# Kernel tuning notes

Measured on AMD Instinct MI355X. Metric: run time of the kernel, lower is better.

Reference implementation:

```python
import jax, jax.numpy as jnp
import numpy as np

N_CLOSEST = 16
OBJECTNESS_THRESH = 0.75


def _masked_softmax(att, mask):
    # softmax over axis 1 restricted to mask; rows with empty mask -> all zeros
    neg = jnp.where(mask, att, -jnp.inf)
    m = jnp.max(neg, axis=1, keepdims=True)
    m = jnp.where(jnp.isfinite(m), m, 0.0)
    e = jnp.where(mask, jnp.exp(att - m), 0.0)
    d = jnp.sum(e, axis=1, keepdims=True)
    return jnp.where(d > 0, e / jnp.maximum(d, 1e-30), 0.0)


def _forward(aggregated_vote_features, ref_obj_features, objectness_scores,
             ref_center_label, aggregated_vote_xyz, emb_table, init_emb,
             W_enc_att, b_enc_att, W_dec_att, b_dec_att, w_full_att, b_full_att,
             W_ih, b_ih, W_hh, b_hh, W_init_h, b_init_h, W_init_c, b_init_c,
             W_fbeta, b_fbeta, W_fc, b_fc, lang_indices, lang_len):
    B, K, VD = aggregated_vote_features.shape
    T = lang_indices.shape[1]

    # --- objectness + distance (top-k closest) masking ---
    objness = jax.nn.softmax(objectness_scores, axis=-1)[:, :, -1]      # [B,K]
    omask = objness > OBJECTNESS_THRESH
    dist = jnp.linalg.norm(ref_center_label[:, None, :] - aggregated_vote_xyz, axis=2)
    dist = jnp.where(omask, dist, jnp.inf)
    closest = -jax.lax.top_k(-dist, N_CLOSEST)[0]                        # k smallest
    max_d = jnp.max(closest, axis=1, keepdims=True)
    object_mask = omask & (dist <= max_d)                                # [B,K]

    enc = aggregated_vote_features                                       # [B,K,VD]
    init_in = jnp.concatenate([enc.mean(axis=1), ref_obj_features], axis=1)
    h0 = init_in @ W_init_h.T + b_init_h                                 # [B,D]
    c0 = init_in @ W_init_c.T + b_init_c

    # encoder attention projection is constant over timesteps
    att1 = jnp.einsum('bkv,av->bka', enc, W_enc_att) + b_enc_att         # [B,K,A]

    # teacher-forcing inputs: <unk> init embedding then caption embeddings
    E = init_emb.shape[-1]
    emb = jnp.concatenate(
        [jnp.broadcast_to(init_emb, (B, E))[:, None, :], emb_table[lang_indices]],
        axis=1)                                                          # [B,T+1,E]
    emb_steps = jnp.swapaxes(emb[:, :T], 0, 1)                           # [T,B,E]
    t_steps = jnp.arange(T)

    def step(carry, xs):
        h, c = carry
        emb_t, t = xs
        # attention
        att2 = h @ W_dec_att.T + b_dec_att                               # [B,A]
        att = jax.nn.relu(att1 + att2[:, None, :]) @ w_full_att + b_full_att[0]  # [B,K]
        alpha = _masked_softmax(att, object_mask)
        awe = jnp.einsum('bkv,bk->bv', enc, alpha)                       # [B,VD]
        gate = jax.nn.sigmoid(h @ W_fbeta.T + b_fbeta)
        awe = gate * awe
        # LSTMCell (torch gate order i,f,g,o)
        x = jnp.concatenate([emb_t, awe, ref_obj_features], axis=1)      # [B,E+VD+OD]
        gates = x @ W_ih.T + b_ih + h @ W_hh.T + b_hh
        i, f, g, o = jnp.split(gates, 4, axis=1)
        c_new = jax.nn.sigmoid(f) * c + jax.nn.sigmoid(i) * jnp.tanh(g)
        h_new = jax.nn.sigmoid(o) * jnp.tanh(c_new)
        # only samples with length > t are decoded (masked equivalent of batch_size_t)
        active = (t < lang_len)[:, None]
        preds = jnp.where(active, h_new @ W_fc.T + b_fc, 0.0)            # [B,V]
        alpha_o = jnp.where(active, alpha, 0.0)
        h = jnp.where(active, h_new, h)
        c = jnp.where(active, c_new, c)
        return (h, c), (preds, alpha_o)

    _, (preds_seq, alpha_seq) = jax.lax.scan(step, (h0, c0), (emb_steps, t_steps))
    predictions = jnp.transpose(preds_seq, (1, 2, 0))                    # [B,V,T]
    alphas = jnp.transpose(alpha_seq, (1, 0, 2))                         # [B,T,K]
    return predictions, alphas, object_mask


def setup_inputs() -> dict:
    key = jax.random.key(0)
    ks = jax.random.split(key, 20)
    B, K, VD, OD, E, A, D, V, T = 128, 128, 128, 256, 300, 512, 512, 4000, 32
    ENC = VD + OD

    def rn(k, shape, s=1.0):
        return jax.random.normal(k, shape, jnp.float32) * s

    return {
        'aggregated_vote_features': rn(ks[0], (B, K, VD)),
        'ref_obj_features': rn(ks[1], (B, OD)),
        'objectness_scores': rn(ks[2], (B, K, 2)),
        'ref_center_label': rn(ks[3], (B, 3)),
        'aggregated_vote_xyz': rn(ks[4], (B, K, 3)),
        'lang_indices': jax.random.randint(ks[5], (B, T), 0, V),
        'lang_len': jax.random.randint(ks[6], (B,), 1, T + 1),
        'emb_table': rn(ks[7], (V, E), 0.1),
        'init_emb': rn(ks[8], (1, E), 0.1),
        'W_enc_att': rn(ks[9], (A, VD), 0.05), 'b_enc_att': jnp.zeros((A,)),
        'W_dec_att': rn(ks[10], (A, D), 0.05), 'b_dec_att': jnp.zeros((A,)),
        'w_full_att': rn(ks[11], (A,), 0.05), 'b_full_att': jnp.zeros((1,)),
        'W_ih': rn(ks[12], (4 * D, E + ENC), 0.05), 'b_ih': jnp.zeros((4 * D,)),
        'W_hh': rn(ks[13], (4 * D, D), 0.05), 'b_hh': jnp.zeros((4 * D,)),
        'W_init_h': rn(ks[14], (D, ENC), 0.05), 'b_init_h': jnp.zeros((D,)),
        'W_init_c': rn(ks[15], (D, ENC), 0.05), 'b_init_c': jnp.zeros((D,)),
        'W_fbeta': rn(ks[16], (VD, D), 0.05), 'b_fbeta': jnp.zeros((VD,)),
        'W_fc': rn(ks[17], (V, D), 0.1), 'b_fc': jnp.zeros((V,)),
    }


def reference(aggregated_vote_features, ref_obj_features, objectness_scores,
              ref_center_label, aggregated_vote_xyz, lang_indices, lang_len,
              emb_table, init_emb, W_enc_att, b_enc_att, W_dec_att, b_dec_att,
              w_full_att, b_full_att, W_ih, b_ih, W_hh, b_hh, W_init_h, b_init_h,
              W_init_c, b_init_c, W_fbeta, b_fbeta, W_fc, b_fc):
    return _forward(aggregated_vote_features, ref_obj_features, objectness_scores,
                    ref_center_label, aggregated_vote_xyz, emb_table, init_emb,
                    W_enc_att, b_enc_att, W_dec_att, b_dec_att, w_full_att, b_full_att,
                    W_ih, b_ih, W_hh, b_hh, W_init_h, b_init_h, W_init_c, b_init_c,
                    W_fbeta, b_fbeta, W_fc, b_fc, lang_indices, lang_len)
```

## Files before the change

### kernel.cpp

```cpp
#include <hip/hip_runtime.h>
#include <hip/hip_bf16.h>
#include <math.h>

#define XKTOT 1196
#define XKP   1216

typedef unsigned short u16;
typedef short bf16x8 __attribute__((ext_vector_type(8)));
typedef float f32x4 __attribute__((ext_vector_type(4)));

static __device__ __forceinline__ float sigmoidf_(float x){ return 1.f/(1.f+expf(-x)); }
static __device__ __forceinline__ u16 f2bf(float x){ __hip_bfloat16 h = __float2bfloat16(x); return *reinterpret_cast<u16*>(&h); }
static __device__ __forceinline__ float bf2f(u16 u){ __hip_bfloat16 h; *reinterpret_cast<u16*>(&h) = u; return __bfloat162float(h); }

__global__ __launch_bounds__(256) void k_transpose(const float* __restrict__ in,
                                                   float* __restrict__ out, int R, int C) {
  __shared__ float tile[32][33];
  int c0 = blockIdx.x * 32, r0 = blockIdx.y * 32;
  int tx = threadIdx.x & 31, ty = threadIdx.x >> 5;
  for (int i = 0; i < 32; i += 8) {
    int r = r0 + ty + i, c = c0 + tx;
    tile[ty + i][tx] = (r < R && c < C) ? in[(size_t)r * C + c] : 0.f;
  }
  __syncthreads();
  for (int i = 0; i < 32; i += 8) {
    int c = c0 + ty + i, r = r0 + tx;
    if (c < C && r < R) out[(size_t)c * R + r] = tile[tx][ty + i];
  }
}

__global__ __launch_bounds__(256) void k_cvt(const float* __restrict__ in,
                                             u16* __restrict__ out, int n) {
  for (int i = blockIdx.x * 256 + threadIdx.x; i < n; i += gridDim.x * 256)
    out[i] = f2bf(in[i]);
}

__global__ __launch_bounds__(256) void k_wcat_split(const float* __restrict__ W_ih,
                                                    const float* __restrict__ W_hh,
                                                    u16* __restrict__ Whi,
                                                    u16* __restrict__ Wlo) {
  int np = blockIdx.x;
  int d = np >> 2, g = np & 3;
  int j = g * 512 + d;
  for (int c = threadIdx.x; c < XKP; c += 256) {
    float v;
    if (c < 684)        v = W_ih[(size_t)j * 684 + c];
    else if (c < 1196)  v = W_hh[(size_t)j * 512 + (c - 684)];
    else                v = 0.f;
    u16 hi = f2bf(v);
    u16 lo = f2bf(v - bf2f(hi));
    Whi[(size_t)np * XKP + c] = hi;
    Wlo[(size_t)np * XKP + c] = lo;
  }
}

__global__ __launch_bounds__(128) void k_mask(const float* __restrict__ objs,
                                              const float* __restrict__ rcl,
                                              const float* __restrict__ avx,
                                              const float* __restrict__ enc,
                                              float* __restrict__ maskf,
                                              float* __restrict__ encmean,
                                              float* __restrict__ out_mask) {
  int b = blockIdx.x, k = threadIdx.x;
  __shared__ float dsh[128];
  __shared__ float maxd;
  float s0 = objs[(size_t)(b * 128 + k) * 2 + 0];
  float s1 = objs[(size_t)(b * 128 + k) * 2 + 1];
  float mx = fmaxf(s0, s1);
  float e0 = expf(s0 - mx), e1 = expf(s1 - mx);
  float p  = e1 / (e0 + e1);
  bool om  = p > 0.75f;
  float dx = rcl[b * 3 + 0] - avx[(size_t)(b * 128 + k) * 3 + 0];
  float dy = rcl[b * 3 + 1] - avx[(size_t)(b * 128 + k) * 3 + 1];
  float dz = rcl[b * 3 + 2] - avx[(size_t)(b * 128 + k) * 3 + 2];
  float dist = sqrtf(dx * dx + dy * dy + dz * dz);
  float dm = om ? dist : INFINITY;
  dsh[k] = dm;
  __syncthreads();
  float v = dm; int clt = 0, cle = 0;
  for (int j = 0; j < 128; j++) { float o = dsh[j]; clt += (o < v); cle += (o <= v); }
  if (clt < 16 && cle >= 16) maxd = v;
  __syncthreads();
  bool msk = om && (dm <= maxd);
  maskf[b * 128 + k]    = msk ? 1.f : 0.f;
  out_mask[b * 128 + k] = msk ? 1.f : 0.f;
  float s = 0.f;
  for (int kk = 0; kk < 128; kk++) s += enc[(size_t)(b * 128 + kk) * 128 + k];
  encmean[b * 128 + k] = s * (1.f / 128.f);
}

__global__ __launch_bounds__(512) void k_init(const float* __restrict__ encm,
                                              const float* __restrict__ rof,
                                              const float* __restrict__ wihT,
                                              const float* __restrict__ wicT,
                                              const float* __restrict__ bh,
                                              const float* __restrict__ bc,
                                              float* __restrict__ h, float* __restrict__ c,
                                              u16* __restrict__ hb16) {
  int b = blockIdx.x, d = threadIdx.x;
  __shared__ float xin[384];
  if (d < 128) xin[d] = encm[b * 128 + d];
  else if (d < 384) xin[d] = rof[(size_t)b * 256 + (d - 128)];
  __syncthreads();
  float ah = bh[d], ac = bc[d];
  for (int i = 0; i < 384; i++) {
    float x = xin[i];
    ah += x * wihT[(size_t)i * 512 + d];
    ac += x * wicT[(size_t)i * 512 + d];
  }
  size_t idx = (size_t)b * 512 + d;
  h[idx] = ah;
  c[idx] = ac;
  hb16[idx] = f2bf(ah);
}

__global__ __launch_bounds__(256) void k_att1m(const u16* __restrict__ enc16,
                                               const u16* __restrict__ We16,
                                               const float* __restrict__ b_enc,
                                               float* __restrict__ att1) {
  int w = threadIdx.x >> 6, lane = threadIdx.x & 63;
  int gw = blockIdx.x * 4 + w;
  int nt = gw & 15, mt = gw >> 4;
  int m0 = mt * 32, n0 = nt * 32;
  int rc = lane & 15, kb = lane >> 4;
  const bf16x8* a0 = (const bf16x8*)(enc16 + (size_t)(m0 + rc) * 128) + kb;
  const bf16x8* a1 = (const bf16x8*)(enc16 + (size_t)(m0 + 16 + rc) * 128) + kb;
  const bf16x8* b0 = (const bf16x8*)(We16 + (size_t)(n0 + rc) * 128) + kb;
  const bf16x8* b1 = (const bf16x8*)(We16 + (size_t)(n0 + 16 + rc) * 128) + kb;
  f32x4 z = {0.f, 0.f, 0.f, 0.f};
  f32x4 acc00 = z, acc01 = z, acc10 = z, acc11 = z;
#pragma unroll
  for (int kk = 0; kk < 4; kk++) {
    bf16x8 av0 = a0[kk * 4], av1 = a1[kk * 4];
    bf16x8 bv0 = b0[kk * 4], bv1 = b1[kk * 4];
    acc00 = __builtin_amdgcn_mfma_f32_16x16x32_bf16(av0, bv0, acc00, 0, 0, 0);
    acc01 = __builtin_amdgcn_mfma_f32_16x16x32_bf16(av0, bv1, acc01, 0, 0, 0);
    acc10 = __builtin_amdgcn_mfma_f32_16x16x32_bf16(av1, bv0, acc10, 0, 0, 0);
    acc11 = __builtin_amdgcn_mfma_f32_16x16x32_bf16(av1, bv1, acc11, 0, 0, 0);
  }
  int col = lane & 15, rbase = (lane >> 4) * 4;
#pragma unroll
  for (int r = 0; r < 4; r++) {
    int r0g = m0 + rbase + r;
    att1[(size_t)r0g * 512 + n0 + col]        = acc00[r] + b_enc[n0 + col];
    att1[(size_t)r0g * 512 + n0 + 16 + col]   = acc01[r] + b_enc[n0 + 16 + col];
    att1[(size_t)(r0g + 16) * 512 + n0 + col]      = acc10[r] + b_enc[n0 + col];
    att1[(size_t)(r0g + 16) * 512 + n0 + 16 + col] = acc11[r] + b_enc[n0 + 16 + col];
  }
}

__global__ __launch_bounds__(512) void k_step_att(
    const float* __restrict__ att1, const float* __restrict__ h,
    const float* __restrict__ wdT, const float* __restrict__ b_dec,
    const float* __restrict__ wfull, const float* __restrict__ bfull,
    const float* __restrict__ enc, const float* __restrict__ maskf,
    const float* __restrict__ wfbT, const float* __restrict__ b_fbeta,
    const float* __restrict__ rof, const float* __restrict__ embt,
    const float* __restrict__ iemb, const int* __restrict__ lidx,
    const int* __restrict__ llen, u16* __restrict__ Xhi, u16* __restrict__ Xlo,
    float* __restrict__ alphas_out, int t) {
  int b = blockIdx.x, tid = threadIdx.x;
  __shared__ float hs[512], att2[512], wf[512], attk[128], alph[128], awes[128];
  __shared__ float red1[2], red2[2];
  hs[tid] = h[(size_t)b * 512 + tid];
  wf[tid] = wfull[tid];
  __syncthreads();
  {
    float acc = b_dec[tid];
    for (int i = 0; i < 512; i++) acc += hs[i] * wdT[(size_t)i * 512 + tid];
    att2[tid] = acc;
  }
  __syncthreads();
  int k = tid >> 2, j = tid & 3;
  {
    const float4* a1 = (const float4*)(att1 + (size_t)(b * 128 + k) * 512 + j * 128);
    float s = 0.f;
#pragma unroll 4
    for (int i = 0; i < 32; i++) {
      float4 v = a1[i];
      int base = j * 128 + i * 4;
      s += fmaxf(v.x + att2[base + 0], 0.f) * wf[base + 0];
      s += fmaxf(v.y + att2[base + 1], 0.f) * wf[base + 1];
      s += fmaxf(v.z + att2[base + 2], 0.f) * wf[base + 2];
      s += fmaxf(v.w + att2[base + 3], 0.f) * wf[base + 3];
    }
    s += __shfl_xor(s, 1);
    s += __shfl_xor(s, 2);
    if (j == 0) attk[k] = s + bfull[0];
  }
  __syncthreads();
  float mk = 0.f, av = 0.f;
  if (tid < 128) { mk = maskf[b * 128 + tid]; av = attk[tid]; }
  float nv = (tid < 128 && mk != 0.f) ? av : -INFINITY;
  float wm = nv;
#pragma unroll
  for (int o = 32; o > 0; o >>= 1) wm = fmaxf(wm, __shfl_xor(wm, o));
  if (tid < 128 && (tid & 63) == 0) red1[tid >> 6] = wm;
  __syncthreads();
  float m = fmaxf(red1[0], red1[1]);
  float e = 0.f;
  if (tid < 128 && mk != 0.f) e = expf(av - m);
  float sred = e;
#pragma unroll
  for (int o = 32; o > 0; o >>= 1) sred += __shfl_xor(sred, o);
  if (tid < 128 && (tid & 63) == 0) red2[tid >> 6] = sred;
  __syncthreads();
  float dsum = red2[0] + red2[1];
  float alpha = (dsum > 0.f) ? e / fmaxf(dsum, 1e-30f) : 0.f;
  int active = t < llen[b];
  if (tid < 128) {
    alph[tid] = alpha;
    alphas_out[(size_t)(b * 32 + t) * 128 + tid] = active ? alpha : 0.f;
  }
  __syncthreads();
  float awe_v = 0.f;
  if (tid < 128) {
    for (int kk = 0; kk < 128; kk++)
      awe_v += alph[kk] * enc[(size_t)(b * 128 + kk) * 128 + tid];
  }
  {
    int v = tid >> 2;
    float g = 0.f;
    for (int ii = 0; ii < 128; ii++) {
      int i = j * 128 + ii;
      g += hs[i] * wfbT[(size_t)i * 128 + v];
    }
    g += __shfl_xor(g, 1);
    g += __shfl_xor(g, 2);
    if (j == 0) attk[v] = sigmoidf_(g + b_fbeta[v]);
  }
  __syncthreads();
  if (tid < 128) awes[tid] = awe_v * attk[tid];
  __syncthreads();
  const float* esrc = (t == 0) ? iemb : (embt + (size_t)lidx[b * 32 + (t - 1)] * 300);
  for (int c = tid; c < XKP; c += 512) {
    float val;
    if (c < 300)       val = esrc[c];
    else if (c < 428)  val = awes[c - 300];
    else if (c < 684)  val = rof[(size_t)b * 256 + (c - 428)];
    else if (c < 1196) val = hs[c - 684];
    else               val = 0.f;
    u16 hi = f2bf(val);
    Xhi[(size_t)b * XKP + c] = hi;
    Xlo[(size_t)b * XKP + c] = f2bf(val - bf2f(hi));
  }
}

__global__ __launch_bounds__(256) void k_gates(const u16* __restrict__ Xhi,
                                               const u16* __restrict__ Xlo,
                                               const u16* __restrict__ Whi,
                                               const u16* __restrict__ Wlo,
                                               const float* __restrict__ b_ih,
                                               const float* __restrict__ b_hh,
                                               const int* __restrict__ llen,
                                               float* __restrict__ h, float* __restrict__ c,
                                               u16* __restrict__ hb16, int t) {
  int w = threadIdx.x >> 6, lane = threadIdx.x & 63;
  int mt = blockIdx.x >> 5;
  int nt = (blockIdx.x & 31) * 4 + w;
  int m0 = mt * 16, n0 = nt * 16;
  int rc = lane & 15, kb = lane >> 4;
  const bf16x8* aHi = (const bf16x8*)(Xhi + (size_t)(m0 + rc) * XKP) + kb;
  const bf16x8* aLo = (const bf16x8*)(Xlo + (size_t)(m0 + rc) * XKP) + kb;
  const bf16x8* bHi = (const bf16x8*)(Whi + (size_t)(n0 + rc) * XKP) + kb;
  const bf16x8* bLo = (const bf16x8*)(Wlo + (size_t)(n0 + rc) * XKP) + kb;
  f32x4 acc = {0.f, 0.f, 0.f, 0.f};
#pragma unroll 2
  for (int kk = 0; kk < 38; kk++) {
    bf16x8 ah = aHi[kk * 4], al = aLo[kk * 4];
    bf16x8 bh = bHi[kk * 4], bl = bLo[kk * 4];
    acc = __builtin_amdgcn_mfma_f32_16x16x32_bf16(ah, bh, acc, 0, 0, 0);
    acc = __builtin_amdgcn_mfma_f32_16x16x32_bf16(al, bh, acc, 0, 0, 0);
    acc = __builtin_amdgcn_mfma_f32_16x16x32_bf16(ah, bl, acc, 0, 0, 0);
  }
  __shared__ float tile[4][16][17];
#pragma unroll
  for (int r = 0; r < 4; r++) tile[w][(lane >> 4) * 4 + r][lane & 15] = acc[r];
  __syncthreads();
  int lb = lane & 15, ld = lane >> 4;
  int b = m0 + lb, d = nt * 4 + ld;
  if (t < llen[b]) {
    float g4[4];
#pragma unroll
    for (int g = 0; g < 4; g++) {
      int jj = g * 512 + d;
      g4[g] = tile[w][lb][ld * 4 + g] + b_ih[jj] + b_hh[jj];
    }
    float i_ = sigmoidf_(g4[0]);
    float f_ = sigmoidf_(g4[1]);
    float gg = tanhf(g4[2]);
    float o_ = sigmoidf_(g4[3]);
    size_t idx = (size_t)b * 512 + d;
    float cn = f_ * c[idx] + i_ * gg;
    float hn = o_ * tanhf(cn);
    c[idx] = cn;
    h[idx] = hn;
    hb16[idx] = f2bf(hn);
  }
}

__global__ __launch_bounds__(256) void k_fc(const u16* __restrict__ hb16,
                                            const u16* __restrict__ Wfc16,
                                            const float* __restrict__ b_fc,
                                            const int* __restrict__ llen,
                                            float* __restrict__ dst, int t, int direct) {
  int w = threadIdx.x >> 6, lane = threadIdx.x & 63;
  int gw = blockIdx.x * 4 + w;
  int mt = gw & 7, nt = gw >> 3;
  int m0 = mt * 16, n0 = nt * 16;
  int rc = lane & 15, kb = lane >> 4;
  const bf16x8* aP = (const bf16x8*)(hb16 + (size_t)(m0 + rc) * 512) + kb;
  const bf16x8* bP = (const bf16x8*)(Wfc16 + (size_t)(n0 + rc) * 512) + kb;
  f32x4 acc = {0.f, 0.f, 0.f, 0.f};
#pragma unroll 4
  for (int kk = 0; kk < 16; kk++)
    acc = __builtin_amdgcn_mfma_f32_16x16x32_bf16(aP[kk * 4], bP[kk * 4], acc, 0, 0, 0);
  int col = lane & 15, rbase = (lane >> 4) * 4;
  int v = n0 + col;
  float bias = b_fc[v];
#pragma unroll
  for (int r = 0; r < 4; r++) {
    int b = m0 + rbase + r;
    float val = (t < llen[b]) ? (acc[r] + bias) : 0.f;
    if (direct) dst[((size_t)b * 4000 + v) * 32 + t] = val;
    else        dst[((size_t)(t * 128 + b)) * 4000 + v] = val;
  }
}

__global__ __launch_bounds__(256) void k_out_tr(const float* __restrict__ predsT,
                                                float* __restrict__ out) {
  __shared__ float tile[32][33];
  int b = blockIdx.y, v0 = blockIdx.x * 32;
  int tx = threadIdx.x & 31, ty = threadIdx.x >> 5;
  for (int i = 0; i < 32; i += 8) {
    int tt = ty + i;
    tile[tt][tx] = predsT[((size_t)tt * 128 + b) * 4000 + v0 + tx];
  }
  __syncthreads();
  for (int i = 0; i < 32; i += 8) {
    int v = v0 + ty + i;
    out[((size_t)b * 4000 + v) * 32 + tx] = tile[tx][ty + i];
  }
}

extern "C" void kernel_launch(void* const* d_in, const int* in_sizes, int n_in,
                              void* d_out, int out_size, void* d_ws, size_t ws_size,
                              hipStream_t stream) {
  (void)in_sizes; (void)n_in; (void)out_size;
  const float* avf   = (const float*)d_in[0];
  const float* rof   = (const float*)d_in[1];
  const float* objs  = (const float*)d_in[2];
  const float* rcl   = (const float*)d_in[3];
  const float* avx   = (const float*)d_in[4];
  const int*   lidx  = (const int*)d_in[5];
  const int*   llen  = (const int*)d_in[6];
  const float* embt  = (const float*)d_in[7];
  const float* iemb  = (const float*)d_in[8];
  const float* W_enc = (const float*)d_in[9];
  const float* b_enc = (const float*)d_in[10];
  const float* W_dec = (const float*)d_in[11];
  const float* b_dec = (const float*)d_in[12];
  const float* wfull = (const float*)d_in[13];
  const float* bfull = (const float*)d_in[14];
  const float* W_ih  = (const float*)d_in[15];
  const float* b_ih  = (const float*)d_in[16];
  const float* W_hh  = (const float*)d_in[17];
  const float* b_hh  = (const float*)d_in[18];
  const float* W_inh = (const float*)d_in[19];
  const float* b_inh = (const float*)d_in[20];
  const float* W_inc = (const float*)d_in[21];
  const float* b_inc = (const float*)d_in[22];
  const float* W_fb  = (const float*)d_in[23];
  const float* b_fb  = (const float*)d_in[24];
  const float* W_fc  = (const float*)d_in[25];
  const float* b_fc  = (const float*)d_in[26];

  float* ws = (float*)d_ws;
  size_t f = 0;
  auto A8 = [&](size_t n) { size_t o = f; f += (n + 63) & ~(size_t)63; return o; };
  float* att1  = ws + A8((size_t)128 * 128 * 512);
  float* wdT   = ws + A8(512 * 512);
  float* wihT  = ws + A8(384 * 512);
  float* wicT  = ws + A8(384 * 512);
  float* wfbT  = ws + A8(512 * 128);
  float* hbuf  = ws + A8(128 * 512);
  float* cbuf  = ws + A8(128 * 512);
  float* maskf = ws + A8(128 * 128);
  float* encm  = ws + A8(128 * 128);
  u16*   Xhi   = (u16*)(ws + A8((size_t)128 * XKP / 2));
  u16*   Xlo   = (u16*)(ws + A8((size_t)128 * XKP / 2));
  u16*   WcatHi= (u16*)(ws + A8((size_t)2048 * XKP / 2));
  u16*   WcatLo= (u16*)(ws + A8((size_t)2048 * XKP / 2));
  u16*   enc16 = (u16*)(ws + A8((size_t)128 * 128 * 128 / 2));
  u16*   We16  = (u16*)(ws + A8((size_t)512 * 128 / 2));
  u16*   Wfc16 = (u16*)(ws + A8((size_t)4000 * 512 / 2));
  u16*   hb16  = (u16*)(ws + A8((size_t)128 * 512 / 2));
  float* predsT= ws + A8((size_t)32 * 128 * 4000);
  bool useT = ws_size >= f * sizeof(float);

  float* out_pred  = (float*)d_out;
  float* out_alpha = out_pred + (size_t)16384000;
  float* out_mask  = out_alpha + (size_t)524288;

  k_transpose<<<dim3(16, 16), 256, 0, stream>>>(W_dec, wdT, 512, 512);
  k_transpose<<<dim3(12, 16), 256, 0, stream>>>(W_inh, wihT, 512, 384);
  k_transpose<<<dim3(12, 16), 256, 0, stream>>>(W_inc, wicT, 512, 384);
  k_transpose<<<dim3(16, 4),  256, 0, stream>>>(W_fb, wfbT, 128, 512);
  k_wcat_split<<<2048, 256, 0, stream>>>(W_ih, W_hh, WcatHi, WcatLo);
  k_cvt<<<2048, 256, 0, stream>>>(avf, enc16, 128 * 128 * 128);
  k_cvt<<<256,  256, 0, stream>>>(W_enc, We16, 512 * 128);
  k_cvt<<<2048, 256, 0, stream>>>(W_fc, Wfc16, 4000 * 512);
  k_mask<<<128, 128, 0, stream>>>(objs, rcl, avx, avf, maskf, encm, out_mask);
  k_init<<<128, 512, 0, stream>>>(encm, rof, wihT, wicT, b_inh, b_inc, hbuf, cbuf, hb16);
  k_att1m<<<2048, 256, 0, stream>>>(enc16, We16, b_enc, att1);

  for (int t = 0; t < 32; t++) {
    k_step_att<<<128, 512, 0, stream>>>(att1, hbuf, wdT, b_dec, wfull, bfull,
        avf, maskf, wfbT, b_fb, rof, embt, iemb, lidx, llen, Xhi, Xlo, out_alpha, t);
    k_gates<<<256, 256, 0, stream>>>(Xhi, Xlo, WcatHi, WcatLo, b_ih, b_hh, llen,
                                     hbuf, cbuf, hb16, t);
    k_fc<<<500, 256, 0, stream>>>(hb16, Wfc16, b_fc, llen,
                                  useT ? predsT : out_pred, t, useT ? 0 : 1);
  }
  if (useT) k_out_tr<<<dim3(125, 128), 256, 0, stream>>>(predsT, out_pred);
}
```

Baseline: 2.435 ms.

## Fuse per-timestep decoder kernels into one cooperative persistent kernel with grid syncs

Replaces the 96 per-step launches (attention, gates, fc) and the final transpose with a single cooperative kernel of 256 blocks. Each step is separated by grid.sync. The decoder-attention projection now runs as a bf16 MFMA GEMM instead of a scalar FP32 loop. The fc output of step t-1 is overlapped with the att2 GEMM of step t. This cuts launch overhead and reduces the work done per block, but it relies on grid-wide barriers, runs at limited occupancy, and lowers att2 precision to bf16.

```diff
diff --git a/kernel.cpp b/kernel.cpp
--- a/kernel.cpp
+++ b/kernel.cpp
@@ -1,9 +1,11 @@
 #include <hip/hip_runtime.h>
 #include <hip/hip_bf16.h>
+#include <hip/hip_cooperative_groups.h>
 #include <math.h>
 
-#define XKTOT 1196
-#define XKP   1216
+namespace cg = cooperative_groups;
+
+#define XKP 1216
 
 typedef unsigned short u16;
 typedef short bf16x8 __attribute__((ext_vector_type(8)));
@@ -149,197 +151,253 @@
   }
 }
 
-__global__ __launch_bounds__(512) void k_step_att(
-    const float* __restrict__ att1, const float* __restrict__ h,
-    const float* __restrict__ wdT, const float* __restrict__ b_dec,
-    const float* __restrict__ wfull, const float* __restrict__ bfull,
-    const float* __restrict__ enc, const float* __restrict__ maskf,
-    const float* __restrict__ wfbT, const float* __restrict__ b_fbeta,
-    const float* __restrict__ rof, const float* __restrict__ embt,
-    const float* __restrict__ iemb, const int* __restrict__ lidx,
-    const int* __restrict__ llen, u16* __restrict__ Xhi, u16* __restrict__ Xlo,
-    float* __restrict__ alphas_out, int t) {
-  int b = blockIdx.x, tid = threadIdx.x;
-  __shared__ float hs[512], att2[512], wf[512], attk[128], alph[128], awes[128];
-  __shared__ float red1[2], red2[2];
-  hs[tid] = h[(size_t)b * 512 + tid];
-  wf[tid] = wfull[tid];
-  __syncthreads();
+struct DecArgs {
+  const float* att1;
+  const u16*   Wdec16;
+  const float* b_dec;
+  const float* wfull;
+  const float* bfull;
+  const float* avf;
+  const float* maskf;
+  const float* wfbT;
+  const float* b_fb;
+  const float* rof;
+  const float* embt;
+  const float* iemb;
+  const int*   lidx;
+  const int*   llen;
+  const u16*   WcatHi;
+  const u16*   WcatLo;
+  const float* b_ih;
+  const float* b_hh;
+  const u16*   Wfc16;
+  const float* b_fc;
+  float* hbuf; float* cbuf; u16* hb16;
+  u16* Xhi; u16* Xlo;
+  float* att2s;
+  float* predsT;
+  float* out_alpha;
+  float* out_pred;
+  int direct;
+};
+
+__global__ __launch_bounds__(256) void k_decode(DecArgs A) {
+  cg::grid_group grid = cg::this_grid();
+  const int tid = threadIdx.x;
+  const int w = tid >> 6, lane = tid & 63;
+  const int gw = blockIdx.x * 4 + w;
+  const int rc = lane & 15, kb = lane >> 4;
+
+  __shared__ float hs[512], a2s[512], wf[512];
+  __shared__ float attk[128], alph[128], gts[128], awes[128];
+  __shared__ float red[8];
+  __shared__ float ttile[32][33];
+
+  for (int t = 0; t < 32; ++t) {
+    if (gw < 256) {
+      int mt = gw & 7, nt = gw >> 3;
+      int m0 = mt * 16, n0 = nt * 16;
+      const bf16x8* aP = (const bf16x8*)(A.hb16 + (size_t)(m0 + rc) * 512) + kb;
+      const bf16x8* bP = (const bf16x8*)(A.Wdec16 + (size_t)(n0 + rc) * 512) + kb;
+      f32x4 acc = {0.f, 0.f, 0.f, 0.f};
+#pragma unroll
+      for (int kk = 0; kk < 16; kk++)
+        acc = __builtin_amdgcn_mfma_f32_16x16x32_bf16(aP[kk * 4], bP[kk * 4], acc, 0, 0, 0);
+      int col = lane & 15, rb = (lane >> 4) * 4;
+      float bias = A.b_dec[n0 + col];
+#pragma unroll
+      for (int r = 0; r < 4; r++)
+        A.att2s[(size_t)(m0 + rb + r) * 512 + n0 + col] = acc[r] + bias;
+    } else if (t > 0) {
+      int tp = t - 1;
+      for (int tile = gw - 256; tile < 2000; tile += 768) {
+        int mt = tile & 7, nt = tile >> 3;
+        int m0 = mt * 16, n0 = nt * 16;
+        const bf16x8* aP = (const bf16x8*)(A.hb16 + (size_t)(m0 + rc) * 512) + kb;
+        const bf16x8* bP = (const bf16x8*)(A.Wfc16 + (size_t)(n0 + rc) * 512) + kb;
+        f32x4 acc = {0.f, 0.f, 0.f, 0.f};
+#pragma unroll
+        for (int kk = 0; kk < 16; kk++)
+          acc = __builtin_amdgcn_mfma_f32_16x16x32_bf16(aP[kk * 4], bP[kk * 4], acc, 0, 0, 0);
+        int col = lane & 15, rb = (lane >> 4) * 4;
+        int v = n0 + col;
+        float bias = A.b_fc[v];
+#pragma unroll
+        for (int r = 0; r < 4; r++) {
+          int b = m0 + rb + r;
+          float val = (tp < A.llen[b]) ? (acc[r] + bias) : 0.f;
+          if (A.direct) A.out_pred[((size_t)b * 4000 + v) * 32 + tp] = val;
+          else          A.predsT[((size_t)(tp * 128 + b)) * 4000 + v] = val;
+        }
+      }
+    }
+    grid.sync();
+
+    if (blockIdx.x < 128) {
+      int b = blockIdx.x;
+      hs[tid] = A.hbuf[(size_t)b * 512 + tid];
+      hs[tid + 256] = A.hbuf[(size_t)b * 512 + 256 + tid];
+      a2s[tid] = A.att2s[(size_t)b * 512 + tid];
+      a2s[tid + 256] = A.att2s[(size_t)b * 512 + 256 + tid];
+      wf[tid] = A.wfull[tid];
+      wf[tid + 256] = A.wfull[tid + 256];
+      __syncthreads();
+      {
+        int k = tid >> 1, half = tid & 1;
+        const float4* a1 = (const float4*)(A.att1 + ((size_t)(b * 128 + k)) * 512 + half * 256);
+        float s = 0.f;
+#pragma unroll 4
+        for (int i = 0; i < 64; i++) {
+          float4 v = a1[i];
+          int base = half * 256 + i * 4;
+          s += fmaxf(v.x + a2s[base + 0], 0.f) * wf[base + 0];
+          s += fmaxf(v.y + a2s[base + 1], 0.f) * wf[base + 1];
+          s += fmaxf(v.z + a2s[base + 2], 0.f) * wf[base + 2];
+          s += fmaxf(v.w + a2s[base + 3], 0.f) * wf[base + 3];
+        }
+        s += __shfl_xor(s, 1);
+        if (half == 0) attk[k] = s + A.bfull[0];
+      }
+      __syncthreads();
+      float mk = 0.f, av = 0.f;
+      if (tid < 128) { mk = A.maskf[b * 128 + tid]; av = attk[tid]; }
+      float nv = (tid < 128 && mk != 0.f) ? av : -INFINITY;
+      float wm = nv;
+#pragma unroll
+      for (int o = 32; o > 0; o >>= 1) wm = fmaxf(wm, __shfl_xor(wm, o));
+      if (tid < 128 && lane == 0) red[w] = wm;
+      __syncthreads();
+      float m = fmaxf(red[0], red[1]);
+      float e = (tid < 128 && mk != 0.f) ? expf(av - m) : 0.f;
+      float sr = e;
+#pragma unroll
+      for (int o = 32; o > 0; o >>= 1) sr += __shfl_xor(sr, o);
+      if (tid < 128 && lane == 0) red[4 + w] = sr;
+      __syncthreads();
+      float dsum = red[4] + red[5];
+      float alpha = (dsum > 0.f) ? e / fmaxf(dsum, 1e-30f) : 0.f;
+      int active = t < A.llen[b];
+      if (tid < 128) {
+        alph[tid] = alpha;
+        A.out_alpha[((size_t)b * 32 + t) * 128 + tid] = active ? alpha : 0.f;
+      }
+      __syncthreads();
+      float awe_v = 0.f;
+      if (tid < 128) {
+        for (int kk = 0; kk < 128; kk++)
+          awe_v += alph[kk] * A.avf[((size_t)b * 128 + kk) * 128 + tid];
+      }
+      {
+        int v = tid >> 1, half = tid & 1;
+        float g = 0.f;
+        for (int ii = 0; ii < 256; ii++) {
+          int i = half * 256 + ii;
+          g += hs[i] * A.wfbT[(size_t)i * 128 + v];
+        }
+        g += __shfl_xor(g, 1);
+        if (half == 0) gts[v] = sigmoidf_(g + A.b_fb[v]);
+      }
+      __syncthreads();
+      if (tid < 128) awes[tid] = awe_v * gts[tid];
+      __syncthreads();
+      const float* esrc = (t == 0) ? A.iemb : (A.embt + (size_t)A.lidx[b * 32 + (t - 1)] * 300);
+      for (int c = tid; c < XKP; c += 256) {
+        float val;
+        if (c < 300)       val = esrc[c];
+        else if (c < 428)  val = awes[c - 300];
+        else if (c < 684)  val = A.rof[(size_t)b * 256 + (c - 428)];
+        else if (c < 1196) val = hs[c - 684];
+        else               val = 0.f;
+        u16 hi = f2bf(val);
+        A.Xhi[(size_t)b * XKP + c] = hi;
+        A.Xlo[(size_t)b * XKP + c] = f2bf(val - bf2f(hi));
+      }
+    }
+    grid.sync();
+
+    {
+      int mt = gw >> 7, ntp = gw & 127;
+      int m0 = mt * 16, n0 = ntp * 16;
+      const bf16x8* aHi = (const bf16x8*)(A.Xhi + (size_t)(m0 + rc) * XKP) + kb;
+      const bf16x8* aLo = (const bf16x8*)(A.Xlo + (size_t)(m0 + rc) * XKP) + kb;
+      const bf16x8* bHi = (const bf16x8*)(A.WcatHi + (size_t)(n0 + rc) * XKP) + kb;
+      const bf16x8* bLo = (const bf16x8*)(A.WcatLo + (size_t)(n0 + rc) * XKP) + kb;
+      f32x4 acc = {0.f, 0.f, 0.f, 0.f};
+#pragma unroll 2
+      for (int kk = 0; kk < 38; kk++) {
+        bf16x8 ah = aHi[kk * 4], al = aLo[kk * 4];
+        bf16x8 bh = bHi[kk * 4], bl = bLo[kk * 4];
+        acc = __builtin_amdgcn_mfma_f32_16x16x32_bf16(ah, bh, acc, 0, 0, 0);
+        acc = __builtin_amdgcn_mfma_f32_16x16x32_bf16(al, bh, acc, 0, 0, 0);
+        acc = __builtin_amdgcn_mfma_f32_16x16x32_bf16(ah, bl, acc, 0, 0, 0);
+      }
+      int col = lane & 15;
+      int d = ntp * 4 + (col >> 2);
+      int baseL = lane & ~3;
+#pragma unroll
+      for (int r = 0; r < 4; r++) {
+        int b = m0 + (lane >> 4) * 4 + r;
+        float g0 = __shfl(acc[r], baseL + 0);
+        float g1 = __shfl(acc[r], baseL + 1);
+        float g2 = __shfl(acc[r], baseL + 2);
+        float g3 = __shfl(acc[r], baseL + 3);
+        if ((lane & 3) == 0 && t < A.llen[b]) {
+          float i_ = sigmoidf_(g0 + A.b_ih[d]        + A.b_hh[d]);
+          float f_ = sigmoidf_(g1 + A.b_ih[512 + d]  + A.b_hh[512 + d]);
+          float gg = tanhf   (g2 + A.b_ih[1024 + d] + A.b_hh[1024 + d]);
+          float o_ = sigmoidf_(g3 + A.b_ih[1536 + d] + A.b_hh[1536 + d]);
+          size_t idx = (size_t)b * 512 + d;
+          float cn = f_ * A.cbuf[idx] + i_ * gg;
+          float hn = o_ * tanhf(cn);
+          A.cbuf[idx] = cn;
+          A.hbuf[idx] = hn;
+          A.hb16[idx] = f2bf(hn);
+        }
+      }
+    }
+    grid.sync();
+  }
+
   {
-    float acc = b_dec[tid];
-    for (int i = 0; i < 512; i++) acc += hs[i] * wdT[(size_t)i * 512 + tid];
-    att2[tid] = acc;
-  }
-  __syncthreads();
-  int k = tid >> 2, j = tid & 3;
-  {
-    const float4* a1 = (const float4*)(att1 + (size_t)(b * 128 + k) * 512 + j * 128);
-    float s = 0.f;
-#pragma unroll 4
-    for (int i = 0; i < 32; i++) {
-      float4 v = a1[i];
-      int base = j * 128 + i * 4;
-      s += fmaxf(v.x + att2[base + 0], 0.f) * wf[base + 0];
-      s += fmaxf(v.y + att2[base + 1], 0.f) * wf[base + 1];
-      s += fmaxf(v.z + att2[base + 2], 0.f) * wf[base + 2];
-      s += fmaxf(v.w + att2[base + 3], 0.f) * wf[base + 3];
+    int tp = 31;
+    for (int tile = gw; tile < 2000; tile += 1024) {
+      int mt = tile & 7, nt = tile >> 3;
+      int m0 = mt * 16, n0 = nt * 16;
+      const bf16x8* aP = (const bf16x8*)(A.hb16 + (size_t)(m0 + rc) * 512) + kb;
+      const bf16x8* bP = (const bf16x8*)(A.Wfc16 + (size_t)(n0 + rc) * 512) + kb;
+      f32x4 acc = {0.f, 0.f, 0.f, 0.f};
+#pragma unroll
+      for (int kk = 0; kk < 16; kk++)
+        acc = __builtin_amdgcn_mfma_f32_16x16x32_bf16(aP[kk * 4], bP[kk * 4], acc, 0, 0, 0);
+      int col = lane & 15, rb = (lane >> 4) * 4;
+      int v = n0 + col;
+      float bias = A.b_fc[v];
+#pragma unroll
+      for (int r = 0; r < 4; r++) {
+        int b = m0 + rb + r;
+        float val = (tp < A.llen[b]) ? (acc[r] + bias) : 0.f;
+        if (A.direct) A.out_pred[((size_t)b * 4000 + v) * 32 + tp] = val;
+        else          A.predsT[((size_t)(tp * 128 + b)) * 4000 + v] = val;
+      }
     }
-    s += __shfl_xor(s, 1);
-    s += __shfl_xor(s, 2);
-    if (j == 0) attk[k] = s + bfull[0];
-  }
-  __syncthreads();
-  float mk = 0.f, av = 0.f;
-  if (tid < 128) { mk = maskf[b * 128 + tid]; av = attk[tid]; }
-  float nv = (tid < 128 && mk != 0.f) ? av : -INFINITY;
-  float wm = nv;
-#pragma unroll
-  for (int o = 32; o > 0; o >>= 1) wm = fmaxf(wm, __shfl_xor(wm, o));
-  if (tid < 128 && (tid & 63) == 0) red1[tid >> 6] = wm;
-  __syncthreads();
-  float m = fmaxf(red1[0], red1[1]);
-  float e = 0.f;
-  if (tid < 128 && mk != 0.f) e = expf(av - m);
-  float sred = e;
-#pragma unroll
-  for (int o = 32; o > 0; o >>= 1) sred += __shfl_xor(sred, o);
-  if (tid < 128 && (tid & 63) == 0) red2[tid >> 6] = sred;
-  __syncthreads();
-  float dsum = red2[0] + red2[1];
-  float alpha = (dsum > 0.f) ? e / fmaxf(dsum, 1e-30f) : 0.f;
-  int active = t < llen[b];
-  if (tid < 128) {
-    alph[tid] = alpha;
-    alphas_out[(size_t)(b * 32 + t) * 128 + tid] = active ? alpha : 0.f;
-  }
-  __syncthreads();
-  float awe_v = 0.f;
-  if (tid < 128) {
-    for (int kk = 0; kk < 128; kk++)
-      awe_v += alph[kk] * enc[(size_t)(b * 128 + kk) * 128 + tid];
-  }
-  {
-    int v = tid >> 2;
-    float g = 0.f;
-    for (int ii = 0; ii < 128; ii++) {
-      int i = j * 128 + ii;
-      g += hs[i] * wfbT[(size_t)i * 128 + v];
+  }
+  if (!A.direct) {
+    grid.sync();
+    for (int tile = blockIdx.x; tile < 16000; tile += 256) {
+      int vt = tile >> 7, b = tile & 127;
+      int v0 = vt * 32;
+      int tx = tid & 31, ty = tid >> 5;
+      __syncthreads();
+      for (int i = 0; i < 32; i += 8) {
+        int tt = ty + i;
+        ttile[tt][tx] = A.predsT[((size_t)tt * 128 + b) * 4000 + v0 + tx];
+      }
+      __syncthreads();
+      for (int i = 0; i < 32; i += 8) {
+        int v = v0 + ty + i;
+        A.out_pred[((size_t)b * 4000 + v) * 32 + tx] = ttile[tx][ty + i];
+      }
     }
-    g += __shfl_xor(g, 1);
-    g += __shfl_xor(g, 2);
-    if (j == 0) attk[v] = sigmoidf_(g + b_fbeta[v]);
-  }
-  __syncthreads();
-  if (tid < 128) awes[tid] = awe_v * attk[tid];
-  __syncthreads();
-  const float* esrc = (t == 0) ? iemb : (embt + (size_t)lidx[b * 32 + (t - 1)] * 300);
-  for (int c = tid; c < XKP; c += 512) {
-    float val;
-    if (c < 300)       val = esrc[c];
-    else if (c < 428)  val = awes[c - 300];
-    else if (c < 684)  val = rof[(size_t)b * 256 + (c - 428)];
-    else if (c < 1196) val = hs[c - 684];
-    else               val = 0.f;
-    u16 hi = f2bf(val);
-    Xhi[(size_t)b * XKP + c] = hi;
-    Xlo[(size_t)b * XKP + c] = f2bf(val - bf2f(hi));
-  }
-}
-
-__global__ __launch_bounds__(256) void k_gates(const u16* __restrict__ Xhi,
-                                               const u16* __restrict__ Xlo,
-                                               const u16* __restrict__ Whi,
-                                               const u16* __restrict__ Wlo,
-                                               const float* __restrict__ b_ih,
-                                               const float* __restrict__ b_hh,
-                                               const int* __restrict__ llen,
-                                               float* __restrict__ h, float* __restrict__ c,
-                                               u16* __restrict__ hb16, int t) {
-  int w = threadIdx.x >> 6, lane = threadIdx.x & 63;
-  int mt = blockIdx.x >> 5;
-  int nt = (blockIdx.x & 31) * 4 + w;
-  int m0 = mt * 16, n0 = nt * 16;
-  int rc = lane & 15, kb = lane >> 4;
-  const bf16x8* aHi = (const bf16x8*)(Xhi + (size_t)(m0 + rc) * XKP) + kb;
-  const bf16x8* aLo = (const bf16x8*)(Xlo + (size_t)(m0 + rc) * XKP) + kb;
-  const bf16x8* bHi = (const bf16x8*)(Whi + (size_t)(n0 + rc) * XKP) + kb;
-  const bf16x8* bLo = (const bf16x8*)(Wlo + (size_t)(n0 + rc) * XKP) + kb;
-  f32x4 acc = {0.f, 0.f, 0.f, 0.f};
-#pragma unroll 2
-  for (int kk = 0; kk < 38; kk++) {
-    bf16x8 ah = aHi[kk * 4], al = aLo[kk * 4];
-    bf16x8 bh = bHi[kk * 4], bl = bLo[kk * 4];
-    acc = __builtin_amdgcn_mfma_f32_16x16x32_bf16(ah, bh, acc, 0, 0, 0);
-    acc = __builtin_amdgcn_mfma_f32_16x16x32_bf16(al, bh, acc, 0, 0, 0);
-    acc = __builtin_amdgcn_mfma_f32_16x16x32_bf16(ah, bl, acc, 0, 0, 0);
-  }
-  __shared__ float tile[4][16][17];
-#pragma unroll
-  for (int r = 0; r < 4; r++) tile[w][(lane >> 4) * 4 + r][lane & 15] = acc[r];
-  __syncthreads();
-  int lb = lane & 15, ld = lane >> 4;
-  int b = m0 + lb, d = nt * 4 + ld;
-  if (t < llen[b]) {
-    float g4[4];
-#pragma unroll
-    for (int g = 0; g < 4; g++) {
-      int jj = g * 512 + d;
-      g4[g] = tile[w][lb][ld * 4 + g] + b_ih[jj] + b_hh[jj];
-    }
-    float i_ = sigmoidf_(g4[0]);
-    float f_ = sigmoidf_(g4[1]);
-    float gg = tanhf(g4[2]);
-    float o_ = sigmoidf_(g4[3]);
-    size_t idx = (size_t)b * 512 + d;
-    float cn = f_ * c[idx] + i_ * gg;
-    float hn = o_ * tanhf(cn);
-    c[idx] = cn;
-    h[idx] = hn;
-    hb16[idx] = f2bf(hn);
-  }
-}
-
-__global__ __launch_bounds__(256) void k_fc(const u16* __restrict__ hb16,
-                                            const u16* __restrict__ Wfc16,
-                                            const float* __restrict__ b_fc,
-                                            const int* __restrict__ llen,
-                                            float* __restrict__ dst, int t, int direct) {
-  int w = threadIdx.x >> 6, lane = threadIdx.x & 63;
-  int gw = blockIdx.x * 4 + w;
-  int mt = gw & 7, nt = gw >> 3;
-  int m0 = mt * 16, n0 = nt * 16;
-  int rc = lane & 15, kb = lane >> 4;
-  const bf16x8* aP = (const bf16x8*)(hb16 + (size_t)(m0 + rc) * 512) + kb;
-  const bf16x8* bP = (const bf16x8*)(Wfc16 + (size_t)(n0 + rc) * 512) + kb;
-  f32x4 acc = {0.f, 0.f, 0.f, 0.f};
-#pragma unroll 4
-  for (int kk = 0; kk < 16; kk++)
-    acc = __builtin_amdgcn_mfma_f32_16x16x32_bf16(aP[kk * 4], bP[kk * 4], acc, 0, 0, 0);
-  int col = lane & 15, rbase = (lane >> 4) * 4;
-  int v = n0 + col;
-  float bias = b_fc[v];
-#pragma unroll
-  for (int r = 0; r < 4; r++) {
-    int b = m0 + rbase + r;
-    float val = (t < llen[b]) ? (acc[r] + bias) : 0.f;
-    if (direct) dst[((size_t)b * 4000 + v) * 32 + t] = val;
-    else        dst[((size_t)(t * 128 + b)) * 4000 + v] = val;
-  }
-}
-
-__global__ __launch_bounds__(256) void k_out_tr(const float* __restrict__ predsT,
-                                                float* __restrict__ out) {
-  __shared__ float tile[32][33];
-  int b = blockIdx.y, v0 = blockIdx.x * 32;
-  int tx = threadIdx.x & 31, ty = threadIdx.x >> 5;
-  for (int i = 0; i < 32; i += 8) {
-    int tt = ty + i;
-    tile[tt][tx] = predsT[((size_t)tt * 128 + b) * 4000 + v0 + tx];
-  }
-  __syncthreads();
-  for (int i = 0; i < 32; i += 8) {
-    int v = v0 + ty + i;
-    out[((size_t)b * 4000 + v) * 32 + tx] = tile[tx][ty + i];
   }
 }
 
@@ -379,7 +437,6 @@
   size_t f = 0;
   auto A8 = [&](size_t n) { size_t o = f; f += (n + 63) & ~(size_t)63; return o; };
   float* att1  = ws + A8((size_t)128 * 128 * 512);
-  float* wdT   = ws + A8(512 * 512);
   float* wihT  = ws + A8(384 * 512);
   float* wicT  = ws + A8(384 * 512);
   float* wfbT  = ws + A8(512 * 128);
@@ -387,12 +444,14 @@
   float* cbuf  = ws + A8(128 * 512);
   float* maskf = ws + A8(128 * 128);
   float* encm  = ws + A8(128 * 128);
+  float* att2s = ws + A8(128 * 512);
   u16*   Xhi   = (u16*)(ws + A8((size_t)128 * XKP / 2));
   u16*   Xlo   = (u16*)(ws + A8((size_t)128 * XKP / 2));
   u16*   WcatHi= (u16*)(ws + A8((size_t)2048 * XKP / 2));
   u16*   WcatLo= (u16*)(ws + A8((size_t)2048 * XKP / 2));
   u16*   enc16 = (u16*)(ws + A8((size_t)128 * 128 * 128 / 2));
   u16*   We16  = (u16*)(ws + A8((size_t)512 * 128 / 2));
+  u16*   Wdec16= (u16*)(ws + A8((size_t)512 * 512 / 2));
   u16*   Wfc16 = (u16*)(ws + A8((size_t)4000 * 512 / 2));
   u16*   hb16  = (u16*)(ws + A8((size_t)128 * 512 / 2));
   float* predsT= ws + A8((size_t)32 * 128 * 4000);
@@ -402,25 +461,29 @@
   float* out_alpha = out_pred + (size_t)16384000;
   float* out_mask  = out_alpha + (size_t)524288;
 
-  k_transpose<<<dim3(16, 16), 256, 0, stream>>>(W_dec, wdT, 512, 512);
   k_transpose<<<dim3(12, 16), 256, 0, stream>>>(W_inh, wihT, 512, 384);
   k_transpose<<<dim3(12, 16), 256, 0, stream>>>(W_inc, wicT, 512, 384);
   k_transpose<<<dim3(16, 4),  256, 0, stream>>>(W_fb, wfbT, 128, 512);
   k_wcat_split<<<2048, 256, 0, stream>>>(W_ih, W_hh, WcatHi, WcatLo);
   k_cvt<<<2048, 256, 0, stream>>>(avf, enc16, 128 * 128 * 128);
   k_cvt<<<256,  256, 0, stream>>>(W_enc, We16, 512 * 128);
+  k_cvt<<<512,  256, 0, stream>>>(W_dec, Wdec16, 512 * 512);
   k_cvt<<<2048, 256, 0, stream>>>(W_fc, Wfc16, 4000 * 512);
   k_mask<<<128, 128, 0, stream>>>(objs, rcl, avx, avf, maskf, encm, out_mask);
   k_init<<<128, 512, 0, stream>>>(encm, rof, wihT, wicT, b_inh, b_inc, hbuf, cbuf, hb16);
   k_att1m<<<2048, 256, 0, stream>>>(enc16, We16, b_enc, att1);
 
-  for (int t = 0; t < 32; t++) {
-    k_step_att<<<128, 512, 0, stream>>>(att1, hbuf, wdT, b_dec, wfull, bfull,
-        avf, maskf, wfbT, b_fb, rof, embt, iemb, lidx, llen, Xhi, Xlo, out_alpha, t);
-    k_gates<<<256, 256, 0, stream>>>(Xhi, Xlo, WcatHi, WcatLo, b_ih, b_hh, llen,
-                                     hbuf, cbuf, hb16, t);
-    k_fc<<<500, 256, 0, stream>>>(hb16, Wfc16, b_fc, llen,
-                                  useT ? predsT : out_pred, t, useT ? 0 : 1);
-  }
-  if (useT) k_out_tr<<<dim3(125, 128), 256, 0, stream>>>(predsT, out_pred);
-}
+  DecArgs da;
+  da.att1 = att1; da.Wdec16 = Wdec16; da.b_dec = b_dec;
+  da.wfull = wfull; da.bfull = bfull; da.avf = avf; da.maskf = maskf;
+  da.wfbT = wfbT; da.b_fb = b_fb; da.rof = rof; da.embt = embt; da.iemb = iemb;
+  da.lidx = lidx; da.llen = llen;
+  da.WcatHi = WcatHi; da.WcatLo = WcatLo; da.b_ih = b_ih; da.b_hh = b_hh;
+  da.Wfc16 = Wfc16; da.b_fc = b_fc;
+  da.hbuf = hbuf; da.cbuf = cbuf; da.hb16 = hb16;
+  da.Xhi = Xhi; da.Xlo = Xlo; da.att2s = att2s;
+  da.predsT = predsT; da.out_alpha = out_alpha; da.out_pred = out_pred;
+  da.direct = useT ? 0 : 1;
+  void* kargs[] = { (void*)&da };
+  hipLaunchCooperativeKernel((const void*)k_decode, dim3(256), dim3(256), kargs, 0, stream);
+}
```

Result: slower. 5.042 ms (+107.1%).
